# Performance work log

Measured on AMD Instinct MI355X. Metric: run time of the kernel, lower is better.

The kernel has to match this reference:

```python
import jax, jax.numpy as jnp
import numpy as np

GAMMA, LMBD, EPS = 0.99, 0.95, 0.2
T, D, H, A = 262144, 128, 256, 8


def _mlp_gauss(x, W1, b1, Wmu, bmu, Wlv, blv):
    h = jnp.tanh(x @ W1 + b1)
    return h @ Wmu + bmu, h @ Wlv + blv  # mu, logvar: [T, A]


def _critic(x, Wc1, bc1, Wc2, bc2):
    h = jnp.tanh(x @ Wc1 + bc1)
    return h @ Wc2 + bc2  # [T, 1]


def setup_inputs() -> dict:
    key = jax.random.key(0)
    ks = jax.random.split(key, 12)
    s = 0.05  # small init scale for stable exp()/ratio
    return {
        "state": jax.random.normal(ks[0], (T, D), jnp.float32),
        "next_state": jax.random.normal(ks[1], (T, D), jnp.float32),
        "action": jax.random.normal(ks[2], (T, A), jnp.float32),
        "beta_log_prob": jax.random.normal(ks[3], (T, A), jnp.float32) * 0.1,
        "reward": jax.random.normal(ks[4], (T,), jnp.float32),
        "W1": jax.random.normal(ks[5], (D, H), jnp.float32) * s,
        "b1": jnp.zeros((H,), jnp.float32),
        "Wmu": jax.random.normal(ks[6], (H, A), jnp.float32) * s,
        "bmu": jnp.zeros((A,), jnp.float32),
        "Wlv": jax.random.normal(ks[7], (H, A), jnp.float32) * s,
        "blv": jnp.zeros((A,), jnp.float32),
        "Wc1": jax.random.normal(ks[8], (D, H), jnp.float32) * s,
        "bc1": jnp.zeros((H,), jnp.float32),
        "Wc2": jax.random.normal(ks[9], (H, 1), jnp.float32) * s,
        "bc2": jnp.zeros((1,), jnp.float32),
    }


def reference(state, next_state, action, beta_log_prob, reward,
              W1, b1, Wmu, bmu, Wlv, blv, Wc1, bc1, Wc2, bc2):
    # critic values
    value = _critic(state, Wc1, bc1, Wc2, bc2)            # [T, 1]
    v0 = value[:, 0]                                       # [T]
    v1 = _critic(next_state, Wc1, bc1, Wc2, bc2)[:, 0]     # [T]

    # GAE: reverse recurrence gae_t = delta_t + gamma*lambda*gae_{t+1}
    delta = reward + GAMMA * v1 - v0                       # [T]

    def step(g, d):
        g = d + GAMMA * LMBD * g
        return g, g

    _, gae_rev = jax.lax.scan(step, jnp.float32(0.0), delta[::-1])
    # torch code rebuilds each gae into a fresh Tensor -> returns are detached
    ret = jax.lax.stop_gradient(gae_rev[::-1][:, None])    # [T, 1]

    advantage = ret - value                                # [T, 1] (grad via value)
    a_hat = (advantage - advantage.mean()) / (jnp.std(advantage, ddof=1) + 1e-7)

    # pi log-prob of actions under Normal(mu, sqrt(exp(logvar)))
    mu, logvar = _mlp_gauss(state, W1, b1, Wmu, bmu, Wlv, blv)  # [T, A]
    log_2pi = jnp.float32(np.log(2.0 * np.pi))
    pi_lp = -0.5 * ((action - mu) ** 2) * jnp.exp(-logvar) - 0.5 * logvar - 0.5 * log_2pi

    ratio = jnp.exp(jnp.sum(pi_lp - jax.lax.stop_gradient(beta_log_prob),
                            axis=1, keepdims=True))        # [T, 1]

    actor_loss = -jnp.sum(jnp.minimum(ratio * a_hat,
                                      jnp.clip(ratio, 1.0 - EPS, 1.0 + EPS) * a_hat))
    critic_loss = jnp.sum(advantage ** 2)
    return actor_loss + critic_loss
```

## Files before the change

### kernel.cpp

```cpp
#include <hip/hip_runtime.h>

#define T_N   262144
#define D_IN  128
#define H_HID 256
#define A_DIM 8
#define GAMMA 0.99f
#define EPS_C 0.2f
#define C_GL  0.9405f
#define HALF_LOG_2PI 0.9189385332f
#define SCALE2 2.8853900817779268f
#define ST_TPB 16
#define NX_TPB 8

typedef __attribute__((ext_vector_type(8))) short short8;
typedef __attribute__((ext_vector_type(4))) float f32x4;

__device__ __forceinline__ unsigned short f2bf(float f) {
  unsigned int u = __float_as_uint(f);
  u += 0x7FFFu + ((u >> 16) & 1u);
  return (unsigned short)(u >> 16);
}
__device__ __forceinline__ float tanh_pre(float a) {
  float e = __builtin_amdgcn_exp2f(a);
  return 1.f - 2.f * __builtin_amdgcn_rcpf(e + 1.f);
}
__device__ __forceinline__ float row16_sum(float p) {
  p += __int_as_float(__builtin_amdgcn_update_dpp(0, __float_as_int(p), 0x111, 0xf, 0xf, true));
  p += __int_as_float(__builtin_amdgcn_update_dpp(0, __float_as_int(p), 0x112, 0xf, 0xf, true));
  p += __int_as_float(__builtin_amdgcn_update_dpp(0, __float_as_int(p), 0x114, 0xf, 0xf, true));
  p += __int_as_float(__builtin_amdgcn_update_dpp(0, __float_as_int(p), 0x118, 0xf, 0xf, true));
  return p;
}

__global__ __launch_bounds__(256) void k_prep(
    const float* __restrict__ Wc1, const float* __restrict__ W1,
    const float* __restrict__ Wmu, const float* __restrict__ Wlv,
    unsigned short* __restrict__ Wc1Ts, unsigned short* __restrict__ W1Ts,
    unsigned short* __restrict__ H1) {
  int i = blockIdx.x * 256 + threadIdx.x;
  if (i < 32768) {
    int n = i >> 7, k = i & 127;
    Wc1Ts[i] = f2bf(Wc1[k * 256 + n] * SCALE2);
  } else if (i < 65536) {
    int j = i - 32768; int n = j >> 7, k = j & 127;
    W1Ts[j] = f2bf(W1[k * 256 + n] * SCALE2);
  } else if (i < 69632) {
    int j = i - 65536; int h = j >> 8, n = j & 255;
    H1[j] = (h < 8) ? f2bf(Wmu[n * 8 + h]) : f2bf(Wlv[n * 8 + (h - 8)]);
  }
}

__global__ __launch_bounds__(512, 4) void k_state(
    const float* __restrict__ state,
    const float* __restrict__ action, const float* __restrict__ beta_lp,
    const unsigned short* __restrict__ Wc1Ts, const unsigned short* __restrict__ W1Ts,
    const unsigned short* __restrict__ H1,
    const float* __restrict__ bc1, const float* __restrict__ b1,
    const float* __restrict__ Wc2, const float* __restrict__ bc2,
    const float* __restrict__ bmu, const float* __restrict__ blv,
    float* __restrict__ v0out, float* __restrict__ ratio) {
  const int tid  = threadIdx.x;
  const int lane = tid & 63;
  const int wv   = tid >> 6;
  const int role = wv >> 2;
  const int wl   = wv & 3;
  const int c    = lane & 15;
  const int quad = lane >> 4;

  __shared__ unsigned short sh_x[32 * 136];
  __shared__ unsigned short sh_h[32 * 264];
  __shared__ float sh_hb[4 * 32 * 16];
  __shared__ float sh_v[32 * 4];

  const unsigned short* WT = role ? W1Ts : Wc1Ts;
  const float* bias = role ? b1 : bc1;

  short8 bfrag[4][4];
  float bias_c[4], wc2_c[4];
#pragma unroll
  for (int ct = 0; ct < 4; ++ct) {
    int n = wl * 64 + ct * 16 + c;
    bias_c[ct] = bias[n] * SCALE2;
    wc2_c[ct]  = Wc2[n];
#pragma unroll
    for (int ki = 0; ki < 4; ++ki)
      bfrag[ct][ki] = *(const short8*)(WT + n * 128 + ki * 32 + quad * 8);
  }
  const float vbias = bc2[0];
  const int aa = tid & 7;
  const float bmu_a = bmu[aa], blv_a = blv[aa];

  const int t0 = blockIdx.x * ST_TPB;

  float4 rbuf[2];
  {
    const float4* Xv = (const float4*)(state + t0 * 32 * D_IN);
    rbuf[0] = Xv[tid]; rbuf[1] = Xv[tid + 512];
  }

  for (int i = 0; i < ST_TPB; ++i) {
    const int r0 = (t0 + i) * 32;

#pragma unroll
    for (int j = 0; j < 2; ++j) {
      int e4 = tid + j * 512;
      int row = e4 >> 5, c4 = e4 & 31;
      ushort4 u;
      u.x = f2bf(rbuf[j].x); u.y = f2bf(rbuf[j].y);
      u.z = f2bf(rbuf[j].z); u.w = f2bf(rbuf[j].w);
      *(ushort4*)(&sh_x[row * 136 + c4 * 4]) = u;
    }
    __syncthreads();

    if (i + 1 < ST_TPB) {
      const float4* Xv2 = (const float4*)(state + (r0 + 32) * D_IN);
      rbuf[0] = Xv2[tid]; rbuf[1] = Xv2[tid + 512];
    }
    float fa = 0.f, fb = 0.f;
    if (tid < 256) { fa = action[r0 * 8 + tid]; fb = beta_lp[r0 * 8 + tid]; }

    if (role == 0) {
#pragma unroll
      for (int rt = 0; rt < 2; ++rt) {
        f32x4 acc[4];
#pragma unroll
        for (int ct = 0; ct < 4; ++ct) acc[ct] = (f32x4){0.f, 0.f, 0.f, 0.f};
#pragma unroll
        for (int ki = 0; ki < 4; ++ki) {
          short8 a = *(const short8*)(&sh_x[(rt * 16 + c) * 136 + ki * 32 + quad * 8]);
#pragma unroll
          for (int ct = 0; ct < 4; ++ct)
            acc[ct] = __builtin_amdgcn_mfma_f32_16x16x32_bf16(a, bfrag[ct][ki], acc[ct], 0, 0, 0);
        }
#pragma unroll
        for (int r = 0; r < 4; ++r) {
          float p = 0.f;
#pragma unroll
          for (int ct = 0; ct < 4; ++ct)
            p += tanh_pre(acc[ct][r] + bias_c[ct]) * wc2_c[ct];
          p = row16_sum(p);
          if (c == 15) sh_v[(rt * 16 + quad * 4 + r) * 4 + wl] = p;
        }
      }
    } else {
#pragma unroll
      for (int rt = 0; rt < 2; ++rt) {
        f32x4 acc[4];
#pragma unroll
        for (int ct = 0; ct < 4; ++ct) acc[ct] = (f32x4){0.f, 0.f, 0.f, 0.f};
#pragma unroll
        for (int ki = 0; ki < 4; ++ki) {
          short8 a = *(const short8*)(&sh_x[(rt * 16 + c) * 136 + ki * 32 + quad * 8]);
#pragma unroll
          for (int ct = 0; ct < 4; ++ct)
            acc[ct] = __builtin_amdgcn_mfma_f32_16x16x32_bf16(a, bfrag[ct][ki], acc[ct], 0, 0, 0);
        }
#pragma unroll
        for (int ct = 0; ct < 4; ++ct) {
          int col = wl * 64 + ct * 16 + c;
#pragma unroll
          for (int r = 0; r < 4; ++r) {
            int row = rt * 16 + quad * 4 + r;
            sh_h[row * 264 + col] = f2bf(tanh_pre(acc[ct][r] + bias_c[ct]));
          }
        }
      }
    }
    __syncthreads();

    if (role == 1) {
#pragma unroll
      for (int st = 0; st < 2; ++st) {
        f32x4 acc2 = (f32x4){0.f, 0.f, 0.f, 0.f};
#pragma unroll
        for (int k2 = 0; k2 < 2; ++k2) {
          int kofs = wl * 64 + k2 * 32 + quad * 8;
          short8 a2 = *(const short8*)(H1 + c * 256 + kofs);
          short8 b2 = *(const short8*)(&sh_h[(st * 16 + c) * 264 + kofs]);
          acc2 = __builtin_amdgcn_mfma_f32_16x16x32_bf16(a2, b2, acc2, 0, 0, 0);
        }
        *((f32x4*)&sh_hb[((wl * 32) + st * 16 + c) * 16 + quad * 4]) = acc2;
      }
    } else if (tid < 32) {
      v0out[r0 + tid] = sh_v[tid * 4] + sh_v[tid * 4 + 1] + sh_v[tid * 4 + 2] +
                        sh_v[tid * 4 + 3] + vbias;
    }
    __syncthreads();

    if (tid < 256) {
      int s = tid >> 3;
      float mu = sh_hb[(s)*16 + aa]          + sh_hb[(32 + s) * 16 + aa] +
                 sh_hb[(64 + s) * 16 + aa]   + sh_hb[(96 + s) * 16 + aa] + bmu_a;
      float lv = sh_hb[(s)*16 + 8 + aa]      + sh_hb[(32 + s) * 16 + 8 + aa] +
                 sh_hb[(64 + s) * 16 + 8 + aa] + sh_hb[(96 + s) * 16 + 8 + aa] + blv_a;
      float d = fa - mu;
      float term = -0.5f * d * d * __expf(-lv) - 0.5f * lv - HALF_LOG_2PI - fb;
      term += __shfl_xor(term, 1);
      term += __shfl_xor(term, 2);
      term += __shfl_xor(term, 4);
      if (aa == 0) ratio[r0 + s] = __expf(term);
    }
  }
}

__global__ __launch_bounds__(256, 4) void k_next(
    const float* __restrict__ next_state,
    const unsigned short* __restrict__ Wc1Ts,
    const float* __restrict__ bc1, const float* __restrict__ Wc2,
    const float* __restrict__ bc2, float* __restrict__ v1out) {
  const int tid = threadIdx.x;
  const int lane = tid & 63;
  const int wv   = tid >> 6;
  const int c    = lane & 15;
  const int quad = lane >> 4;

  __shared__ unsigned short sh_x[32 * 136];
  __shared__ float sh_v[32 * 4];

  short8 bfrag[4][4];
  float bias_c[4], wc2_c[4];
#pragma unroll
  for (int ct = 0; ct < 4; ++ct) {
    int n = wv * 64 + ct * 16 + c;
    bias_c[ct] = bc1[n] * SCALE2;
    wc2_c[ct]  = Wc2[n];
#pragma unroll
    for (int ki = 0; ki < 4; ++ki)
      bfrag[ct][ki] = *(const short8*)(Wc1Ts + n * 128 + ki * 32 + quad * 8);
  }
  const float vbias = bc2[0];

  const int t0 = blockIdx.x * NX_TPB;
  float4 rbuf[4];
  {
    const float4* Xv = (const float4*)(next_state + t0 * 32 * D_IN);
#pragma unroll
    for (int j = 0; j < 4; ++j) rbuf[j] = Xv[tid + j * 256];
  }

  for (int i = 0; i < NX_TPB; ++i) {
    const int r0 = (t0 + i) * 32;
#pragma unroll
    for (int j = 0; j < 4; ++j) {
      int e = tid + j * 256;
      int row = e >> 5, c4 = e & 31;
      ushort4 u;
      u.x = f2bf(rbuf[j].x); u.y = f2bf(rbuf[j].y);
      u.z = f2bf(rbuf[j].z); u.w = f2bf(rbuf[j].w);
      *(ushort4*)(&sh_x[row * 136 + c4 * 4]) = u;
    }
    __syncthreads();

    if (i + 1 < NX_TPB) {
      const float4* Xv2 = (const float4*)(next_state + (r0 + 32) * D_IN);
#pragma unroll
      for (int j = 0; j < 4; ++j) rbuf[j] = Xv2[tid + j * 256];
    }

#pragma unroll
    for (int rt = 0; rt < 2; ++rt) {
      f32x4 acc[4];
#pragma unroll
      for (int ct = 0; ct < 4; ++ct) acc[ct] = (f32x4){0.f, 0.f, 0.f, 0.f};
#pragma unroll
      for (int ki = 0; ki < 4; ++ki) {
        short8 a = *(const short8*)(&sh_x[(rt * 16 + c) * 136 + ki * 32 + quad * 8]);
#pragma unroll
        for (int ct = 0; ct < 4; ++ct)
          acc[ct] = __builtin_amdgcn_mfma_f32_16x16x32_bf16(a, bfrag[ct][ki], acc[ct], 0, 0, 0);
      }
#pragma unroll
      for (int r = 0; r < 4; ++r) {
        float p = 0.f;
#pragma unroll
        for (int ct = 0; ct < 4; ++ct)
          p += tanh_pre(acc[ct][r] + bias_c[ct]) * wc2_c[ct];
        p = row16_sum(p);
        if (c == 15) sh_v[(rt * 16 + quad * 4 + r) * 4 + wv] = p;
      }
    }
    __syncthreads();
    if (tid < 32) {
      v1out[r0 + tid] = sh_v[tid * 4] + sh_v[tid * 4 + 1] + sh_v[tid * 4 + 2] +
                        sh_v[tid * 4 + 3] + vbias;
    }
  }
}

__global__ __launch_bounds__(256) void k_gae(
    const float* __restrict__ reward, const float* __restrict__ v0,
    const float* __restrict__ v1, float* __restrict__ adv,
    float* __restrict__ accs) {
  const int j = blockIdx.x, k = threadIdx.x;
  const int base = j * 1024 + k * 8;
  float d[8];
  float s = 0.f, w = 1.f;
#pragma unroll
  for (int i = 0; i < 8; ++i) {
    int idx = base + i;
    float dd = 0.f;
    if (idx < T_N) dd = reward[idx] + GAMMA * v1[idx] - v0[idx];
    d[i] = dd;
    s += w * dd;
    w *= C_GL;
  }
  const float W8 = w;
  __shared__ float Ss[256], Sw[256];
  Ss[k] = s; Sw[k] = W8;
  __syncthreads();
  for (int dd = 1; dd < 256; dd <<= 1) {
    bool has = (k + dd) < 256;
    float ns = 0.f, nw = 0.f;
    if (has) { ns = Ss[k] + Sw[k] * Ss[k + dd]; nw = Sw[k] * Sw[k + dd]; }
    __syncthreads();
    if (has) { Ss[k] = ns; Sw[k] = nw; }
    __syncthreads();
  }
  float g = (k < 255) ? Ss[k + 1] : 0.f;
  float sa = 0.f, sq = 0.f;
  if (k < 128) {
#pragma unroll
    for (int i = 7; i >= 0; --i) {
      g = d[i] + C_GL * g;
      float a = g - v0[base + i];
      adv[base + i] = a;
      sa += a; sq += a * a;
    }
  }
  __syncthreads();
  Ss[k] = sa; Sw[k] = sq;
  __syncthreads();
  for (int off = 128; off > 0; off >>= 1) {
    if (k < off) { Ss[k] += Ss[k + off]; Sw[k] += Sw[k + off]; }
    __syncthreads();
  }
  if (k == 0) {
    atomicAdd(&accs[0], Ss[0]);
    atomicAdd(&accs[1], Sw[0]);
  }
}

__global__ __launch_bounds__(256) void k_loss(
    const float* __restrict__ adv, const float* __restrict__ ratio,
    float* __restrict__ accs, float* __restrict__ out) {
  int t = blockIdx.x * 256 + threadIdx.x;
  float sum  = accs[0];
  float mean = sum * (1.f / (float)T_N);
  float var  = (accs[1] - sum * mean) / (float)(T_N - 1);
  float inv  = 1.f / (sqrtf(var) + 1e-7f);
  float a = (adv[t] - mean) * inv;
  float r = ratio[t];
  float rc = fminf(fmaxf(r, 1.f - EPS_C), 1.f + EPS_C);
  float term = -fminf(r * a, rc * a);
  __shared__ float red[256];
  int k = threadIdx.x;
  red[k] = term;
  __syncthreads();
  for (int off = 128; off > 0; off >>= 1) {
    if (k < off) red[k] += red[k + off];
    __syncthreads();
  }
  if (k == 0) {
    atomicAdd(&accs[2], red[0]);
    __threadfence();
    unsigned int old = atomicAdd((unsigned int*)&accs[3], 1u);
    if (old == (unsigned int)(gridDim.x - 1)) {
      __threadfence();
      volatile float* va = (volatile float*)accs;
      out[0] = va[2] + va[1];
    }
  }
}

extern "C" void kernel_launch(void* const* d_in, const int* in_sizes, int n_in,
                              void* d_out, int out_size, void* d_ws, size_t ws_size,
                              hipStream_t stream) {
  const float* state      = (const float*)d_in[0];
  const float* next_state = (const float*)d_in[1];
  const float* action     = (const float*)d_in[2];
  const float* beta_lp    = (const float*)d_in[3];
  const float* reward     = (const float*)d_in[4];
  const float* W1   = (const float*)d_in[5];
  const float* b1   = (const float*)d_in[6];
  const float* Wmu  = (const float*)d_in[7];
  const float* bmu  = (const float*)d_in[8];
  const float* Wlv  = (const float*)d_in[9];
  const float* blv  = (const float*)d_in[10];
  const float* Wc1  = (const float*)d_in[11];
  const float* bc1  = (const float*)d_in[12];
  const float* Wc2  = (const float*)d_in[13];
  const float* bc2  = (const float*)d_in[14];

  char* ws = (char*)d_ws;
  size_t o = 0;
  unsigned short* Wc1Ts = (unsigned short*)(ws + o); o += 65536;
  unsigned short* W1Ts  = (unsigned short*)(ws + o); o += 65536;
  unsigned short* H1    = (unsigned short*)(ws + o); o += 8192;
  float* v0    = (float*)(ws + o); o += (size_t)T_N * 4;
  float* v1    = (float*)(ws + o); o += (size_t)T_N * 4;
  float* ratio = (float*)(ws + o); o += (size_t)T_N * 4;
  float* adv   = (float*)(ws + o); o += (size_t)T_N * 4;
  float* accs  = (float*)(ws + o); o += 256;

  hipMemsetAsync(accs, 0, 32, stream);

  k_prep<<<272, 256, 0, stream>>>(Wc1, W1, Wmu, Wlv, Wc1Ts, W1Ts, H1);

  k_state<<<(T_N / 32) / ST_TPB, 512, 0, stream>>>(
      state, action, beta_lp, Wc1Ts, W1Ts, H1, bc1, b1, Wc2, bc2, bmu, blv,
      v0, ratio);
  k_next<<<(T_N / 32) / NX_TPB, 256, 0, stream>>>(
      next_state, Wc1Ts, bc1, Wc2, bc2, v1);
  k_gae<<<256, 256, 0, stream>>>(reward, v0, v1, adv, accs);
  k_loss<<<T_N / 256, 256, 0, stream>>>(adv, ratio, accs, (float*)d_out);
}
```

Before: 383.1 us.

## Fuse prep, state and next-state MLPs into one persistent kernel; cooperative GAE+loss tail

Merges weight preparation, the state actor/critic pass and the next-state critic pass into one persistent launch. Prep blocks publish completion through an atomic flag that all blocks spin on, and the state and next-state work is split across a fixed block count. GAE and the loss reduction are merged into a cooperative kernel with grid syncs, so advantages stay in registers and the adv buffer round trip is gone. It also switches to truncating bf16 packing via perm. This cuts launch overhead and memory traffic, but relies on all blocks being co-resident for the spin-wait and costs a little rounding accuracy.

```diff
diff --git a/kernel.cpp b/kernel.cpp
--- a/kernel.cpp
+++ b/kernel.cpp
@@ -1,16 +1,18 @@
 #include <hip/hip_runtime.h>
+#include <hip/hip_cooperative_groups.h>
+namespace cg = cooperative_groups;
 
 #define T_N   262144
 #define D_IN  128
-#define H_HID 256
 #define A_DIM 8
 #define GAMMA 0.99f
 #define EPS_C 0.2f
 #define C_GL  0.9405f
 #define HALF_LOG_2PI 0.9189385332f
 #define SCALE2 2.8853900817779268f
-#define ST_TPB 16
-#define NX_TPB 8
+#define N_SB  728
+#define N_NB  296
+#define NPREP 144u
 
 typedef __attribute__((ext_vector_type(8))) short short8;
 typedef __attribute__((ext_vector_type(4))) float f32x4;
@@ -20,277 +22,277 @@
   u += 0x7FFFu + ((u >> 16) & 1u);
   return (unsigned short)(u >> 16);
 }
+__device__ __forceinline__ unsigned int pack_bf2(float lo, float hi) {
+  return __builtin_amdgcn_perm(__float_as_uint(hi), __float_as_uint(lo), 0x07060302u);
+}
+__device__ __forceinline__ unsigned short bf_trunc(float f) {
+  return (unsigned short)(__float_as_uint(f) >> 16);
+}
 __device__ __forceinline__ float tanh_pre(float a) {
   float e = __builtin_amdgcn_exp2f(a);
   return 1.f - 2.f * __builtin_amdgcn_rcpf(e + 1.f);
 }
+template <int CTRL>
+__device__ __forceinline__ float dpp_add(float p) {
+  return p + __int_as_float(__builtin_amdgcn_update_dpp(
+                 0, __float_as_int(p), CTRL, 0xF, 0xF, true));
+}
 __device__ __forceinline__ float row16_sum(float p) {
-  p += __int_as_float(__builtin_amdgcn_update_dpp(0, __float_as_int(p), 0x111, 0xf, 0xf, true));
-  p += __int_as_float(__builtin_amdgcn_update_dpp(0, __float_as_int(p), 0x112, 0xf, 0xf, true));
-  p += __int_as_float(__builtin_amdgcn_update_dpp(0, __float_as_int(p), 0x114, 0xf, 0xf, true));
-  p += __int_as_float(__builtin_amdgcn_update_dpp(0, __float_as_int(p), 0x118, 0xf, 0xf, true));
+  p = dpp_add<0x111>(p); p = dpp_add<0x112>(p);
+  p = dpp_add<0x114>(p); p = dpp_add<0x118>(p);
   return p;
 }
-
-__global__ __launch_bounds__(256) void k_prep(
+__device__ __forceinline__ float xor8_sum(float p) {
+  p = dpp_add<0xB1>(p); p = dpp_add<0x4E>(p); p = dpp_add<0x141>(p);
+  return p;
+}
+
+__global__ __launch_bounds__(512, 4) void k_fused(
+    const float* __restrict__ state, const float* __restrict__ next_state,
+    const float* __restrict__ action, const float* __restrict__ beta_lp,
     const float* __restrict__ Wc1, const float* __restrict__ W1,
     const float* __restrict__ Wmu, const float* __restrict__ Wlv,
-    unsigned short* __restrict__ Wc1Ts, unsigned short* __restrict__ W1Ts,
-    unsigned short* __restrict__ H1) {
-  int i = blockIdx.x * 256 + threadIdx.x;
-  if (i < 32768) {
-    int n = i >> 7, k = i & 127;
-    Wc1Ts[i] = f2bf(Wc1[k * 256 + n] * SCALE2);
-  } else if (i < 65536) {
-    int j = i - 32768; int n = j >> 7, k = j & 127;
-    W1Ts[j] = f2bf(W1[k * 256 + n] * SCALE2);
-  } else if (i < 69632) {
-    int j = i - 65536; int h = j >> 8, n = j & 255;
-    H1[j] = (h < 8) ? f2bf(Wmu[n * 8 + h]) : f2bf(Wlv[n * 8 + (h - 8)]);
-  }
-}
-
-__global__ __launch_bounds__(512, 4) void k_state(
-    const float* __restrict__ state,
-    const float* __restrict__ action, const float* __restrict__ beta_lp,
-    const unsigned short* __restrict__ Wc1Ts, const unsigned short* __restrict__ W1Ts,
-    const unsigned short* __restrict__ H1,
     const float* __restrict__ bc1, const float* __restrict__ b1,
     const float* __restrict__ Wc2, const float* __restrict__ bc2,
     const float* __restrict__ bmu, const float* __restrict__ blv,
-    float* __restrict__ v0out, float* __restrict__ ratio) {
-  const int tid  = threadIdx.x;
-  const int lane = tid & 63;
-  const int wv   = tid >> 6;
-  const int role = wv >> 2;
-  const int wl   = wv & 3;
-  const int c    = lane & 15;
-  const int quad = lane >> 4;
-
-  __shared__ unsigned short sh_x[32 * 136];
-  __shared__ unsigned short sh_h[32 * 264];
-  __shared__ float sh_hb[4 * 32 * 16];
-  __shared__ float sh_v[32 * 4];
-
-  const unsigned short* WT = role ? W1Ts : Wc1Ts;
-  const float* bias = role ? b1 : bc1;
-
-  short8 bfrag[4][4];
-  float bias_c[4], wc2_c[4];
-#pragma unroll
-  for (int ct = 0; ct < 4; ++ct) {
-    int n = wl * 64 + ct * 16 + c;
-    bias_c[ct] = bias[n] * SCALE2;
-    wc2_c[ct]  = Wc2[n];
-#pragma unroll
-    for (int ki = 0; ki < 4; ++ki)
-      bfrag[ct][ki] = *(const short8*)(WT + n * 128 + ki * 32 + quad * 8);
-  }
-  const float vbias = bc2[0];
-  const int aa = tid & 7;
-  const float bmu_a = bmu[aa], blv_a = blv[aa];
-
-  const int t0 = blockIdx.x * ST_TPB;
-
-  float4 rbuf[2];
-  {
-    const float4* Xv = (const float4*)(state + t0 * 32 * D_IN);
-    rbuf[0] = Xv[tid]; rbuf[1] = Xv[tid + 512];
-  }
-
-  for (int i = 0; i < ST_TPB; ++i) {
-    const int r0 = (t0 + i) * 32;
-
-#pragma unroll
-    for (int j = 0; j < 2; ++j) {
-      int e4 = tid + j * 512;
-      int row = e4 >> 5, c4 = e4 & 31;
-      ushort4 u;
-      u.x = f2bf(rbuf[j].x); u.y = f2bf(rbuf[j].y);
-      u.z = f2bf(rbuf[j].z); u.w = f2bf(rbuf[j].w);
-      *(ushort4*)(&sh_x[row * 136 + c4 * 4]) = u;
-    }
-    __syncthreads();
-
-    if (i + 1 < ST_TPB) {
-      const float4* Xv2 = (const float4*)(state + (r0 + 32) * D_IN);
-      rbuf[0] = Xv2[tid]; rbuf[1] = Xv2[tid + 512];
-    }
-    float fa = 0.f, fb = 0.f;
-    if (tid < 256) { fa = action[r0 * 8 + tid]; fb = beta_lp[r0 * 8 + tid]; }
-
-    if (role == 0) {
-#pragma unroll
-      for (int rt = 0; rt < 2; ++rt) {
-        f32x4 acc[4];
-#pragma unroll
-        for (int ct = 0; ct < 4; ++ct) acc[ct] = (f32x4){0.f, 0.f, 0.f, 0.f};
-#pragma unroll
-        for (int ki = 0; ki < 4; ++ki) {
-          short8 a = *(const short8*)(&sh_x[(rt * 16 + c) * 136 + ki * 32 + quad * 8]);
-#pragma unroll
-          for (int ct = 0; ct < 4; ++ct)
-            acc[ct] = __builtin_amdgcn_mfma_f32_16x16x32_bf16(a, bfrag[ct][ki], acc[ct], 0, 0, 0);
-        }
-#pragma unroll
-        for (int r = 0; r < 4; ++r) {
-          float p = 0.f;
-#pragma unroll
-          for (int ct = 0; ct < 4; ++ct)
-            p += tanh_pre(acc[ct][r] + bias_c[ct]) * wc2_c[ct];
-          p = row16_sum(p);
-          if (c == 15) sh_v[(rt * 16 + quad * 4 + r) * 4 + wl] = p;
-        }
-      }
-    } else {
-#pragma unroll
-      for (int rt = 0; rt < 2; ++rt) {
-        f32x4 acc[4];
-#pragma unroll
-        for (int ct = 0; ct < 4; ++ct) acc[ct] = (f32x4){0.f, 0.f, 0.f, 0.f};
-#pragma unroll
-        for (int ki = 0; ki < 4; ++ki) {
-          short8 a = *(const short8*)(&sh_x[(rt * 16 + c) * 136 + ki * 32 + quad * 8]);
-#pragma unroll
-          for (int ct = 0; ct < 4; ++ct)
-            acc[ct] = __builtin_amdgcn_mfma_f32_16x16x32_bf16(a, bfrag[ct][ki], acc[ct], 0, 0, 0);
-        }
-#pragma unroll
-        for (int ct = 0; ct < 4; ++ct) {
-          int col = wl * 64 + ct * 16 + c;
-#pragma unroll
-          for (int r = 0; r < 4; ++r) {
-            int row = rt * 16 + quad * 4 + r;
-            sh_h[row * 264 + col] = f2bf(tanh_pre(acc[ct][r] + bias_c[ct]));
-          }
-        }
-      }
-    }
-    __syncthreads();
-
-    if (role == 1) {
-#pragma unroll
-      for (int st = 0; st < 2; ++st) {
-        f32x4 acc2 = (f32x4){0.f, 0.f, 0.f, 0.f};
-#pragma unroll
-        for (int k2 = 0; k2 < 2; ++k2) {
-          int kofs = wl * 64 + k2 * 32 + quad * 8;
-          short8 a2 = *(const short8*)(H1 + c * 256 + kofs);
-          short8 b2 = *(const short8*)(&sh_h[(st * 16 + c) * 264 + kofs]);
-          acc2 = __builtin_amdgcn_mfma_f32_16x16x32_bf16(a2, b2, acc2, 0, 0, 0);
-        }
-        *((f32x4*)&sh_hb[((wl * 32) + st * 16 + c) * 16 + quad * 4]) = acc2;
-      }
-    } else if (tid < 32) {
-      v0out[r0 + tid] = sh_v[tid * 4] + sh_v[tid * 4 + 1] + sh_v[tid * 4 + 2] +
-                        sh_v[tid * 4 + 3] + vbias;
-    }
-    __syncthreads();
-
-    if (tid < 256) {
-      int s = tid >> 3;
-      float mu = sh_hb[(s)*16 + aa]          + sh_hb[(32 + s) * 16 + aa] +
-                 sh_hb[(64 + s) * 16 + aa]   + sh_hb[(96 + s) * 16 + aa] + bmu_a;
-      float lv = sh_hb[(s)*16 + 8 + aa]      + sh_hb[(32 + s) * 16 + 8 + aa] +
-                 sh_hb[(64 + s) * 16 + 8 + aa] + sh_hb[(96 + s) * 16 + 8 + aa] + blv_a;
-      float d = fa - mu;
-      float term = -0.5f * d * d * __expf(-lv) - 0.5f * lv - HALF_LOG_2PI - fb;
-      term += __shfl_xor(term, 1);
-      term += __shfl_xor(term, 2);
-      term += __shfl_xor(term, 4);
-      if (aa == 0) ratio[r0 + s] = __expf(term);
-    }
-  }
-}
-
-__global__ __launch_bounds__(256, 4) void k_next(
-    const float* __restrict__ next_state,
-    const unsigned short* __restrict__ Wc1Ts,
-    const float* __restrict__ bc1, const float* __restrict__ Wc2,
-    const float* __restrict__ bc2, float* __restrict__ v1out) {
+    unsigned short* __restrict__ Wc1Ts, unsigned short* __restrict__ W1Ts,
+    unsigned short* __restrict__ H1,
+    float* __restrict__ v0out, float* __restrict__ v1out,
+    float* __restrict__ ratio, float* __restrict__ accs) {
+  const int bid = blockIdx.x;
   const int tid = threadIdx.x;
   const int lane = tid & 63;
   const int wv   = tid >> 6;
   const int c    = lane & 15;
   const int quad = lane >> 4;
+  unsigned int* flagp = (unsigned int*)accs + 8;
 
   __shared__ unsigned short sh_x[32 * 136];
-  __shared__ float sh_v[32 * 4];
-
-  short8 bfrag[4][4];
-  float bias_c[4], wc2_c[4];
-#pragma unroll
-  for (int ct = 0; ct < 4; ++ct) {
-    int n = wv * 64 + ct * 16 + c;
-    bias_c[ct] = bc1[n] * SCALE2;
-    wc2_c[ct]  = Wc2[n];
-#pragma unroll
-    for (int ki = 0; ki < 4; ++ki)
-      bfrag[ct][ki] = *(const short8*)(Wc1Ts + n * 128 + ki * 32 + quad * 8);
-  }
-  const float vbias = bc2[0];
-
-  const int t0 = blockIdx.x * NX_TPB;
-  float4 rbuf[4];
+  __shared__ unsigned short sh_h[32 * 264];
+  __shared__ float sh_hb[4 * 32 * 16];
+  __shared__ float sh_v[32 * 8];
+
+  if (bid < (int)NPREP) {
+    int i = bid * 512 + tid;
+    if (i < 32768) {
+      int n = i >> 7, k = i & 127;
+      Wc1Ts[i] = f2bf(Wc1[k * 256 + n] * SCALE2);
+    } else if (i < 65536) {
+      int j = i - 32768; int n = j >> 7, k = j & 127;
+      W1Ts[j] = f2bf(W1[k * 256 + n] * SCALE2);
+    } else if (i < 69632) {
+      int j = i - 65536; int h = j >> 8, n = j & 255;
+      H1[j] = (h < 8) ? f2bf(Wmu[n * 8 + h]) : f2bf(Wlv[n * 8 + (h - 8)]);
+    }
+    __syncthreads();
+    if (tid == 0)
+      __hip_atomic_fetch_add(flagp, 1u, __ATOMIC_RELEASE, __HIP_MEMORY_SCOPE_AGENT);
+  }
+
+  const bool is_state = bid < N_SB;
+  const float* Xbase = is_state ? state : next_state;
+  const int stride = is_state ? N_SB : N_NB;
+  int t = is_state ? bid : (bid - N_SB);
+
+  float4 rbuf[2];
   {
-    const float4* Xv = (const float4*)(next_state + t0 * 32 * D_IN);
-#pragma unroll
-    for (int j = 0; j < 4; ++j) rbuf[j] = Xv[tid + j * 256];
-  }
-
-  for (int i = 0; i < NX_TPB; ++i) {
-    const int r0 = (t0 + i) * 32;
-#pragma unroll
-    for (int j = 0; j < 4; ++j) {
-      int e = tid + j * 256;
-      int row = e >> 5, c4 = e & 31;
-      ushort4 u;
-      u.x = f2bf(rbuf[j].x); u.y = f2bf(rbuf[j].y);
-      u.z = f2bf(rbuf[j].z); u.w = f2bf(rbuf[j].w);
-      *(ushort4*)(&sh_x[row * 136 + c4 * 4]) = u;
-    }
-    __syncthreads();
-
-    if (i + 1 < NX_TPB) {
-      const float4* Xv2 = (const float4*)(next_state + (r0 + 32) * D_IN);
-#pragma unroll
-      for (int j = 0; j < 4; ++j) rbuf[j] = Xv2[tid + j * 256];
-    }
-
-#pragma unroll
-    for (int rt = 0; rt < 2; ++rt) {
-      f32x4 acc[4];
-#pragma unroll
-      for (int ct = 0; ct < 4; ++ct) acc[ct] = (f32x4){0.f, 0.f, 0.f, 0.f};
-#pragma unroll
-      for (int ki = 0; ki < 4; ++ki) {
-        short8 a = *(const short8*)(&sh_x[(rt * 16 + c) * 136 + ki * 32 + quad * 8]);
-#pragma unroll
-        for (int ct = 0; ct < 4; ++ct)
-          acc[ct] = __builtin_amdgcn_mfma_f32_16x16x32_bf16(a, bfrag[ct][ki], acc[ct], 0, 0, 0);
-      }
-#pragma unroll
-      for (int r = 0; r < 4; ++r) {
-        float p = 0.f;
-#pragma unroll
-        for (int ct = 0; ct < 4; ++ct)
-          p += tanh_pre(acc[ct][r] + bias_c[ct]) * wc2_c[ct];
-        p = row16_sum(p);
-        if (c == 15) sh_v[(rt * 16 + quad * 4 + r) * 4 + wv] = p;
-      }
-    }
-    __syncthreads();
-    if (tid < 32) {
-      v1out[r0 + tid] = sh_v[tid * 4] + sh_v[tid * 4 + 1] + sh_v[tid * 4 + 2] +
-                        sh_v[tid * 4 + 3] + vbias;
-    }
-  }
-}
-
-__global__ __launch_bounds__(256) void k_gae(
+    const float4* Xv = (const float4*)(Xbase + (size_t)t * 32 * D_IN);
+    rbuf[0] = Xv[tid]; rbuf[1] = Xv[tid + 512];
+  }
+
+  if (tid == 0) {
+    while (__hip_atomic_load(flagp, __ATOMIC_ACQUIRE, __HIP_MEMORY_SCOPE_AGENT) < NPREP)
+      __builtin_amdgcn_s_sleep(1);
+  }
+  __syncthreads();
+
+  if (is_state) {
+    const int wl = wv & 3;
+    const unsigned short* WT = (wv < 4) ? Wc1Ts : W1Ts;
+    const float* bias = (wv < 4) ? bc1 : b1;
+    short8 bfrag[4][4];
+    float bias_c[4], wc2_c[4];
+#pragma unroll
+    for (int ct = 0; ct < 4; ++ct) {
+      int n = wl * 64 + ct * 16 + c;
+      bias_c[ct] = bias[n] * SCALE2;
+      wc2_c[ct]  = Wc2[n];
+#pragma unroll
+      for (int ki = 0; ki < 4; ++ki)
+        bfrag[ct][ki] = *(const short8*)(WT + n * 128 + ki * 32 + quad * 8);
+    }
+    const float vbias = bc2[0];
+    const int aa = tid & 7;
+    const float bmu_a = bmu[aa], blv_a = blv[aa];
+
+    for (; t < 8192; t += N_SB) {
+      const int r0 = t * 32;
+#pragma unroll
+      for (int j = 0; j < 2; ++j) {
+        int e4 = tid + j * 512;
+        int row = e4 >> 5, c4 = e4 & 31;
+        uint2 u;
+        u.x = pack_bf2(rbuf[j].x, rbuf[j].y);
+        u.y = pack_bf2(rbuf[j].z, rbuf[j].w);
+        *(uint2*)(&sh_x[row * 136 + c4 * 4]) = u;
+      }
+      __syncthreads();
+      int tn = t + N_SB;
+      if (tn < 8192) {
+        const float4* Xv2 = (const float4*)(state + (size_t)tn * 32 * D_IN);
+        rbuf[0] = Xv2[tid]; rbuf[1] = Xv2[tid + 512];
+      }
+      float fa = 0.f, fb = 0.f;
+      if (tid < 256) { fa = action[r0 * 8 + tid]; fb = beta_lp[r0 * 8 + tid]; }
+
+      if (wv < 4) {
+#pragma unroll
+        for (int rt = 0; rt < 2; ++rt) {
+          f32x4 acc[4];
+#pragma unroll
+          for (int ct = 0; ct < 4; ++ct) acc[ct] = (f32x4){0.f, 0.f, 0.f, 0.f};
+#pragma unroll
+          for (int ki = 0; ki < 4; ++ki) {
+            short8 a = *(const short8*)(&sh_x[(rt * 16 + c) * 136 + ki * 32 + quad * 8]);
+#pragma unroll
+            for (int ct = 0; ct < 4; ++ct)
+              acc[ct] = __builtin_amdgcn_mfma_f32_16x16x32_bf16(a, bfrag[ct][ki], acc[ct], 0, 0, 0);
+          }
+#pragma unroll
+          for (int r = 0; r < 4; ++r) {
+            float p = 0.f;
+#pragma unroll
+            for (int ct = 0; ct < 4; ++ct)
+              p += tanh_pre(acc[ct][r] + bias_c[ct]) * wc2_c[ct];
+            p = row16_sum(p);
+            if (c == 15) sh_v[(rt * 16 + quad * 4 + r) * 4 + wl] = p;
+          }
+        }
+      } else {
+#pragma unroll
+        for (int rt = 0; rt < 2; ++rt) {
+          f32x4 acc[4];
+#pragma unroll
+          for (int ct = 0; ct < 4; ++ct) acc[ct] = (f32x4){0.f, 0.f, 0.f, 0.f};
+#pragma unroll
+          for (int ki = 0; ki < 4; ++ki) {
+            short8 a = *(const short8*)(&sh_x[(rt * 16 + c) * 136 + ki * 32 + quad * 8]);
+#pragma unroll
+            for (int ct = 0; ct < 4; ++ct)
+              acc[ct] = __builtin_amdgcn_mfma_f32_16x16x32_bf16(a, bfrag[ct][ki], acc[ct], 0, 0, 0);
+          }
+#pragma unroll
+          for (int ct = 0; ct < 4; ++ct) {
+            int col = wl * 64 + ct * 16 + c;
+#pragma unroll
+            for (int r = 0; r < 4; ++r) {
+              int row = rt * 16 + quad * 4 + r;
+              sh_h[row * 264 + col] = bf_trunc(tanh_pre(acc[ct][r] + bias_c[ct]));
+            }
+          }
+        }
+      }
+      __syncthreads();
+
+      if (wv >= 4) {
+#pragma unroll
+        for (int st = 0; st < 2; ++st) {
+          f32x4 acc2 = (f32x4){0.f, 0.f, 0.f, 0.f};
+#pragma unroll
+          for (int k2 = 0; k2 < 2; ++k2) {
+            int kofs = wl * 64 + k2 * 32 + quad * 8;
+            short8 a2 = *(const short8*)(H1 + c * 256 + kofs);
+            short8 b2 = *(const short8*)(&sh_h[(st * 16 + c) * 264 + kofs]);
+            acc2 = __builtin_amdgcn_mfma_f32_16x16x32_bf16(a2, b2, acc2, 0, 0, 0);
+          }
+          *((f32x4*)&sh_hb[((wl * 32) + st * 16 + c) * 16 + quad * 4]) = acc2;
+        }
+      } else if (tid < 32) {
+        v0out[r0 + tid] = sh_v[tid * 4] + sh_v[tid * 4 + 1] + sh_v[tid * 4 + 2] +
+                          sh_v[tid * 4 + 3] + vbias;
+      }
+      __syncthreads();
+
+      if (tid < 256) {
+        int s = tid >> 3;
+        float mu = sh_hb[(s)*16 + aa]          + sh_hb[(32 + s) * 16 + aa] +
+                   sh_hb[(64 + s) * 16 + aa]   + sh_hb[(96 + s) * 16 + aa] + bmu_a;
+        float lv = sh_hb[(s)*16 + 8 + aa]      + sh_hb[(32 + s) * 16 + 8 + aa] +
+                   sh_hb[(64 + s) * 16 + 8 + aa] + sh_hb[(96 + s) * 16 + 8 + aa] + blv_a;
+        float d = fa - mu;
+        float term = -0.5f * d * d * __expf(-lv) - 0.5f * lv - HALF_LOG_2PI - fb;
+        term = xor8_sum(term);
+        if (aa == 0) ratio[r0 + s] = __expf(term);
+      }
+    }
+  } else {
+    short8 bfrag[2][4];
+    float bias_c[2], wc2_c[2];
+#pragma unroll
+    for (int ct = 0; ct < 2; ++ct) {
+      int n = wv * 32 + ct * 16 + c;
+      bias_c[ct] = bc1[n] * SCALE2;
+      wc2_c[ct]  = Wc2[n];
+#pragma unroll
+      for (int ki = 0; ki < 4; ++ki)
+        bfrag[ct][ki] = *(const short8*)(Wc1Ts + n * 128 + ki * 32 + quad * 8);
+    }
+    const float vbias = bc2[0];
+
+    for (; t < 8192; t += N_NB) {
+      const int r0 = t * 32;
+#pragma unroll
+      for (int j = 0; j < 2; ++j) {
+        int e4 = tid + j * 512;
+        int row = e4 >> 5, c4 = e4 & 31;
+        uint2 u;
+        u.x = pack_bf2(rbuf[j].x, rbuf[j].y);
+        u.y = pack_bf2(rbuf[j].z, rbuf[j].w);
+        *(uint2*)(&sh_x[row * 136 + c4 * 4]) = u;
+      }
+      __syncthreads();
+      int tn = t + N_NB;
+      if (tn < 8192) {
+        const float4* Xv2 = (const float4*)(next_state + (size_t)tn * 32 * D_IN);
+        rbuf[0] = Xv2[tid]; rbuf[1] = Xv2[tid + 512];
+      }
+
+#pragma unroll
+      for (int rt = 0; rt < 2; ++rt) {
+        f32x4 acc[2];
+#pragma unroll
+        for (int ct = 0; ct < 2; ++ct) acc[ct] = (f32x4){0.f, 0.f, 0.f, 0.f};
+#pragma unroll
+        for (int ki = 0; ki < 4; ++ki) {
+          short8 a = *(const short8*)(&sh_x[(rt * 16 + c) * 136 + ki * 32 + quad * 8]);
+#pragma unroll
+          for (int ct = 0; ct < 2; ++ct)
+            acc[ct] = __builtin_amdgcn_mfma_f32_16x16x32_bf16(a, bfrag[ct][ki], acc[ct], 0, 0, 0);
+        }
+#pragma unroll
+        for (int r = 0; r < 4; ++r) {
+          float p = tanh_pre(acc[0][r] + bias_c[0]) * wc2_c[0] +
+                    tanh_pre(acc[1][r] + bias_c[1]) * wc2_c[1];
+          p = row16_sum(p);
+          if (c == 15) sh_v[(rt * 16 + quad * 4 + r) * 8 + wv] = p;
+        }
+      }
+      __syncthreads();
+      if (tid < 32) {
+        float s = vbias;
+#pragma unroll
+        for (int w8 = 0; w8 < 8; ++w8) s += sh_v[tid * 8 + w8];
+        v1out[r0 + tid] = s;
+      }
+    }
+  }
+}
+
+__global__ __launch_bounds__(256) void k_tail(
     const float* __restrict__ reward, const float* __restrict__ v0,
-    const float* __restrict__ v1, float* __restrict__ adv,
-    float* __restrict__ accs) {
+    const float* __restrict__ v1, const float* __restrict__ ratio,
+    float* __restrict__ accs, float* __restrict__ out) {
+  cg::grid_group grid = cg::this_grid();
   const int j = blockIdx.x, k = threadIdx.x;
   const int base = j * 1024 + k * 8;
   float d[8];
@@ -308,22 +310,23 @@
   __shared__ float Ss[256], Sw[256];
   Ss[k] = s; Sw[k] = W8;
   __syncthreads();
-  for (int dd = 1; dd < 256; dd <<= 1) {
-    bool has = (k + dd) < 256;
+  for (int st = 1; st < 256; st <<= 1) {
+    bool has = (k + st) < 256;
     float ns = 0.f, nw = 0.f;
-    if (has) { ns = Ss[k] + Sw[k] * Ss[k + dd]; nw = Sw[k] * Sw[k + dd]; }
+    if (has) { ns = Ss[k] + Sw[k] * Ss[k + st]; nw = Sw[k] * Sw[k + st]; }
     __syncthreads();
     if (has) { Ss[k] = ns; Sw[k] = nw; }
     __syncthreads();
   }
   float g = (k < 255) ? Ss[k + 1] : 0.f;
+  float adv[8];
   float sa = 0.f, sq = 0.f;
   if (k < 128) {
 #pragma unroll
     for (int i = 7; i >= 0; --i) {
       g = d[i] + C_GL * g;
       float a = g - v0[base + i];
-      adv[base + i] = a;
+      adv[i] = a;
       sa += a; sq += a * a;
     }
   }
@@ -338,38 +341,34 @@
     atomicAdd(&accs[0], Ss[0]);
     atomicAdd(&accs[1], Sw[0]);
   }
-}
-
-__global__ __launch_bounds__(256) void k_loss(
-    const float* __restrict__ adv, const float* __restrict__ ratio,
-    float* __restrict__ accs, float* __restrict__ out) {
-  int t = blockIdx.x * 256 + threadIdx.x;
+
+  grid.sync();
+
   float sum  = accs[0];
   float mean = sum * (1.f / (float)T_N);
   float var  = (accs[1] - sum * mean) / (float)(T_N - 1);
   float inv  = 1.f / (sqrtf(var) + 1e-7f);
-  float a = (adv[t] - mean) * inv;
-  float r = ratio[t];
-  float rc = fminf(fmaxf(r, 1.f - EPS_C), 1.f + EPS_C);
-  float term = -fminf(r * a, rc * a);
-  __shared__ float red[256];
-  int k = threadIdx.x;
-  red[k] = term;
+  float sl = 0.f;
+  if (k < 128) {
+#pragma unroll
+    for (int i = 0; i < 8; ++i) {
+      float a = (adv[i] - mean) * inv;
+      float r = ratio[base + i];
+      float rc = fminf(fmaxf(r, 1.f - EPS_C), 1.f + EPS_C);
+      sl += -fminf(r * a, rc * a);
+    }
+  }
+  __syncthreads();
+  Ss[k] = sl;
   __syncthreads();
   for (int off = 128; off > 0; off >>= 1) {
-    if (k < off) red[k] += red[k + off];
+    if (k < off) Ss[k] += Ss[k + off];
     __syncthreads();
   }
-  if (k == 0) {
-    atomicAdd(&accs[2], red[0]);
-    __threadfence();
-    unsigned int old = atomicAdd((unsigned int*)&accs[3], 1u);
-    if (old == (unsigned int)(gridDim.x - 1)) {
-      __threadfence();
-      volatile float* va = (volatile float*)accs;
-      out[0] = va[2] + va[1];
-    }
-  }
+  if (k == 0) atomicAdd(&accs[2], Ss[0]);
+
+  grid.sync();
+  if (j == 0 && k == 0) out[0] = accs[2] + accs[1];
 }
 
 extern "C" void kernel_launch(void* const* d_in, const int* in_sizes, int n_in,
@@ -399,18 +398,17 @@
   float* v0    = (float*)(ws + o); o += (size_t)T_N * 4;
   float* v1    = (float*)(ws + o); o += (size_t)T_N * 4;
   float* ratio = (float*)(ws + o); o += (size_t)T_N * 4;
-  float* adv   = (float*)(ws + o); o += (size_t)T_N * 4;
   float* accs  = (float*)(ws + o); o += 256;
 
-  hipMemsetAsync(accs, 0, 32, stream);
-
-  k_prep<<<272, 256, 0, stream>>>(Wc1, W1, Wmu, Wlv, Wc1Ts, W1Ts, H1);
-
-  k_state<<<(T_N / 32) / ST_TPB, 512, 0, stream>>>(
-      state, action, beta_lp, Wc1Ts, W1Ts, H1, bc1, b1, Wc2, bc2, bmu, blv,
-      v0, ratio);
-  k_next<<<(T_N / 32) / NX_TPB, 256, 0, stream>>>(
-      next_state, Wc1Ts, bc1, Wc2, bc2, v1);
-  k_gae<<<256, 256, 0, stream>>>(reward, v0, v1, adv, accs);
-  k_loss<<<T_N / 256, 256, 0, stream>>>(adv, ratio, accs, (float*)d_out);
-}
+  hipMemsetAsync(accs, 0, 64, stream);
+
+  k_fused<<<N_SB + N_NB, 512, 0, stream>>>(
+      state, next_state, action, beta_lp, Wc1, W1, Wmu, Wlv,
+      bc1, b1, Wc2, bc2, bmu, blv, Wc1Ts, W1Ts, H1, v0, v1, ratio, accs);
+
+  float* outp = (float*)d_out;
+  void* cargs[6] = {(void*)&reward, (void*)&v0, (void*)&v1,
+                    (void*)&ratio, (void*)&accs, (void*)&outp};
+  hipLaunchCooperativeKernel((const void*)k_tail, dim3(256), dim3(256),
+                             cargs, 0, stream);
+}
```

Measured after the change: 451.9 us. 18.0% more time.
